# Performance work log

Measured on AMD Instinct MI355X. Metric: run time of the kernel, lower is better.

The kernel has to match this reference:

```python
import jax, jax.numpy as jnp
import numpy as np

B, LQ, LM, D, H = 2, 2048, 2048, 1024, 16
DH = D // H  # 64

def setup_inputs() -> dict:
    key = jax.random.key(0)
    ks = jax.random.split(key, 11)
    s = 0.02
    return {
        "query": jax.random.normal(ks[0], (B, LQ, D), jnp.float32),
        "memory": jax.random.normal(ks[1], (B, LM, D), jnp.float32),
        "memory_bias": jax.random.normal(ks[2], (B, LM), jnp.float32),
        "Wq": jax.random.normal(ks[3], (D, D), jnp.float32) * s,
        "bq": jnp.zeros((D,), jnp.float32),
        "Wk": jax.random.normal(ks[4], (D, D), jnp.float32) * s,
        "bk": jnp.zeros((D,), jnp.float32),
        "Wv": jax.random.normal(ks[5], (D, D), jnp.float32) * s,
        "bv": jnp.zeros((D,), jnp.float32),
        "Wo": jax.random.normal(ks[6], (D, D), jnp.float32) * s,
        "bo": jnp.zeros((D,), jnp.float32),
    }

def reference(query, memory, memory_bias, Wq, bq, Wk, bk, Wv, bv, Wo, bo):
    # QKV projections, split into heads: [B, L, H, DH]
    q = (query @ Wq + bq).reshape(B, LQ, H, DH)
    k = (memory @ Wk + bk).reshape(B, LM, H, DH)
    v = (memory @ Wv + bv).reshape(B, LM, H, DH)
    q = q * (DH ** -0.5)
    # logits: [B, H, Lq, Lk] (matches torch.einsum('btnh,bfnh->bnft', k, q))
    logits = jnp.einsum("bfnh,btnh->bnft", q, k)
    logits = logits + memory_bias[:, None, None, :]  # bias [B, Lm] -> [B,1,1,Lk]
    weights = jax.nn.softmax(logits, axis=-1)
    # dropout omitted (eval / rate 0 for correctness baseline)
    attn = jnp.einsum("bnft,btnh->bfnh", weights, v).reshape(B, LQ, D)
    return attn @ Wo + bo  # [B, Lq, output_depth]
```

## Files before the change

### kernel.cpp

```cpp
#include <hip/hip_runtime.h>
#include <hip/hip_bf16.h>
#include <math.h>


typedef __bf16 bf16;
typedef __bf16 bf16x4 __attribute__((ext_vector_type(4)));
typedef __bf16 bf16x8 __attribute__((ext_vector_type(8)));
typedef float f32x4 __attribute__((ext_vector_type(4)));

#define MFMA16(a, b, c) __builtin_amdgcn_mfma_f32_16x16x32_bf16((a), (b), (c), 0, 0, 0)

__device__ inline float exp2_hw(float x) {
    float r; asm("v_exp_f32 %0, %1" : "=v"(r) : "v"(x)); return r;
}

__device__ inline void gload_lds16(const void* g, void* l) {
    __builtin_amdgcn_global_load_lds(
        (const __attribute__((address_space(1))) void*)g,
        (__attribute__((address_space(3))) void*)l, 16, 0, 0);
}

__global__ __launch_bounds__(256) void prep_kernel(
    const float* __restrict__ query, const float* __restrict__ memory,
    const float* __restrict__ mbias,
    const float* __restrict__ W0, const float* __restrict__ W1,
    const float* __restrict__ W2, const float* __restrict__ W3,
    bf16* __restrict__ Yq, bf16* __restrict__ Ym, float* __restrict__ sbias,
    bf16* __restrict__ T0, bf16* __restrict__ T1,
    bf16* __restrict__ T2, bf16* __restrict__ T3)
{
    __shared__ float Ls[64][65];
    const int t = threadIdx.x;

    if (blockIdx.z == 0) {
        const float* X = blockIdx.y ? memory : query;
        bf16* Y = blockIdx.y ? Ym : Yq;
        const size_t i = ((size_t)blockIdx.x * 256 + t) * 8;
        float4 f0 = *(const float4*)&X[i];
        float4 f1 = *(const float4*)&X[i + 4];
        bf16x8 h;
        h[0] = (bf16)f0.x; h[1] = (bf16)f0.y; h[2] = (bf16)f0.z; h[3] = (bf16)f0.w;
        h[4] = (bf16)f1.x; h[5] = (bf16)f1.y; h[6] = (bf16)f1.z; h[7] = (bf16)f1.w;
        *(bf16x8*)&Y[i] = h;
        return;
    }
    const int x = blockIdx.x;
    if (x == 1024) {
        const int i = blockIdx.y * 2048 + t * 8;
        #pragma unroll
        for (int j = 0; j < 8; ++j) sbias[i + j] = mbias[i + j] * 1.44269504f;
        return;
    }
    if (x > 1024 || blockIdx.y) return;

    const int wsel = x >> 8, sub = x & 255;
    const float* W; bf16* T;
    switch (wsel) {
        case 0:  W = W0; T = T0; break;
        case 1:  W = W1; T = T1; break;
        case 2:  W = W2; T = T2; break;
        default: W = W3; T = T3; break;
    }
    const int n0 = (sub & 15) * 64, k0 = (sub >> 4) * 64;
    const int g = t >> 4, c = (t & 15) * 4;
    #pragma unroll
    for (int p = 0; p < 4; ++p) {
        const int row = p * 16 + g;
        float4 f = *(const float4*)&W[(size_t)(k0 + row) * 1024 + n0 + c];
        Ls[row][c + 0] = f.x; Ls[row][c + 1] = f.y;
        Ls[row][c + 2] = f.z; Ls[row][c + 3] = f.w;
    }
    __syncthreads();
    #pragma unroll
    for (int p = 0; p < 4; ++p) {
        const int n = p * 16 + g;
        bf16x4 h;
        h[0] = (bf16)Ls[c + 0][n]; h[1] = (bf16)Ls[c + 1][n];
        h[2] = (bf16)Ls[c + 2][n]; h[3] = (bf16)Ls[c + 3][n];
        *(bf16x4*)&T[(size_t)(n0 + n) * 1024 + k0 + c] = h;
    }
}

template <typename TO>
__global__ __launch_bounds__(256) void gemm_kernel(
    const bf16* __restrict__ A, const bf16* __restrict__ WT,
    const float* __restrict__ bias, TO* __restrict__ out,
    float alpha, int mode)
{
    __shared__ __align__(16) bf16 As[2][128 * 64];
    __shared__ __align__(16) bf16 Bs[2][64 * 64];

    const int fid = blockIdx.x + (blockIdx.y << 4);
    const int swz = (fid & 7) * 64 + (fid >> 3);
    const int n0 = (swz & 15) * 64;
    const int m0 = (swz >> 4) * 128;

    const int tid = threadIdx.x;
    const int w = tid >> 6, lane = tid & 63;
    const int lr = lane & 15, lg = lane >> 4;
    const int wm = (w >> 1) * 64, wn = (w & 1) * 32;

    const int arow0 = w * 32 + (lane >> 3);
    const int brow0 = w * 16 + (lane >> 3);
    const int sch = lane & 7;

    f32x4 acc[4][2] = {};

    auto stageG = [&](int kt, int bi) {
        #pragma unroll
        for (int p = 0; p < 4; ++p) {
            const int row = arow0 + p * 8;
            const int xc = ((sch ^ (row & 7)) << 3);
            gload_lds16(&A[(size_t)(m0 + row) * 1024 + kt + xc],
                        &As[bi][row * 64 + sch * 8]);
        }
        #pragma unroll
        for (int p = 0; p < 2; ++p) {
            const int row = brow0 + p * 8;
            const int xc = ((sch ^ (row & 7)) << 3);
            gload_lds16(&WT[(size_t)(n0 + row) * 1024 + kt + xc],
                        &Bs[bi][row * 64 + sch * 8]);
        }
    };

    stageG(0, 0);
    __syncthreads();

    int cur = 0;
    #pragma unroll 1
    for (int t = 0; t < 16; ++t) {
        if (t < 15) stageG((t + 1) * 64, cur ^ 1);

        #pragma unroll
        for (int ks = 0; ks < 2; ++ks) {
            const int c = (((ks * 4 + lg) ^ (lr & 7)) << 3);
            bf16x8 af[4], bfv[2];
            #pragma unroll
            for (int mt = 0; mt < 4; ++mt)
                af[mt] = *(const bf16x8*)&As[cur][(wm + mt * 16 + lr) * 64 + c];
            #pragma unroll
            for (int nt = 0; nt < 2; ++nt)
                bfv[nt] = *(const bf16x8*)&Bs[cur][(wn + nt * 16 + lr) * 64 + c];
            #pragma unroll
            for (int nt = 0; nt < 2; ++nt)
                #pragma unroll
                for (int mt = 0; mt < 4; ++mt)
                    acc[mt][nt] = MFMA16(af[mt], bfv[nt], acc[mt][nt]);
        }
        __syncthreads();
        cur ^= 1;
    }

    #pragma unroll
    for (int nt = 0; nt < 2; ++nt) {
        const int n = n0 + wn + nt * 16 + lr;
        const float bv = bias[n];
        #pragma unroll
        for (int mt = 0; mt < 4; ++mt) {
            #pragma unroll
            for (int i = 0; i < 4; ++i) {
                const int m = m0 + wm + mt * 16 + lg * 4 + i;
                const float v = (acc[mt][nt][i] + bv) * alpha;
                if (mode == 0) {
                    out[(size_t)m * 1024 + n] = (TO)v;
                } else {
                    const int b = m >> 11, t2 = m & 2047;
                    out[((size_t)(b << 10) + n) * 2048 + t2] = (TO)v;
                }
            }
        }
    }
}

__global__ __launch_bounds__(256) void gemm_kv_kernel(
    const bf16* __restrict__ A, const bf16* __restrict__ WTk,
    const bf16* __restrict__ WTv, const float* __restrict__ bk,
    const float* __restrict__ bv, bf16* __restrict__ Kout,
    bf16* __restrict__ Vtout)
{
    __shared__ __align__(16) bf16 As[2][128 * 64];
    __shared__ __align__(16) bf16 Bk[2][64 * 64];
    __shared__ __align__(16) bf16 Bv[2][64 * 64];

    const int fid = blockIdx.x + (blockIdx.y << 4);
    const int swz = (fid & 7) * 64 + (fid >> 3);
    const int n0 = (swz & 15) * 64;
    const int m0 = (swz >> 4) * 128;

    const int tid = threadIdx.x;
    const int w = tid >> 6, lane = tid & 63;
    const int lr = lane & 15, lg = lane >> 4;
    const int wm = (w >> 1) * 64, wn = (w & 1) * 32;

    const int arow0 = w * 32 + (lane >> 3);
    const int brow0 = w * 16 + (lane >> 3);
    const int sch = lane & 7;

    f32x4 accK[4][2] = {}, accV[4][2] = {};

    auto stageG = [&](int kt, int bi) {
        #pragma unroll
        for (int p = 0; p < 4; ++p) {
            const int row = arow0 + p * 8;
            const int xc = ((sch ^ (row & 7)) << 3);
            gload_lds16(&A[(size_t)(m0 + row) * 1024 + kt + xc],
                        &As[bi][row * 64 + sch * 8]);
        }
        #pragma unroll
        for (int p = 0; p < 2; ++p) {
            const int row = brow0 + p * 8;
            const int xc = ((sch ^ (row & 7)) << 3);
            gload_lds16(&WTk[(size_t)(n0 + row) * 1024 + kt + xc],
                        &Bk[bi][row * 64 + sch * 8]);
            gload_lds16(&WTv[(size_t)(n0 + row) * 1024 + kt + xc],
                        &Bv[bi][row * 64 + sch * 8]);
        }
    };

    stageG(0, 0);
    __syncthreads();

    int cur = 0;
    #pragma unroll 1
    for (int t = 0; t < 16; ++t) {
        if (t < 15) stageG((t + 1) * 64, cur ^ 1);

        #pragma unroll
        for (int ks = 0; ks < 2; ++ks) {
            const int c = (((ks * 4 + lg) ^ (lr & 7)) << 3);
            bf16x8 af[4], bkf[2], bvf[2];
            #pragma unroll
            for (int mt = 0; mt < 4; ++mt)
                af[mt] = *(const bf16x8*)&As[cur][(wm + mt * 16 + lr) * 64 + c];
            #pragma unroll
            for (int nt = 0; nt < 2; ++nt) {
                bkf[nt] = *(const bf16x8*)&Bk[cur][(wn + nt * 16 + lr) * 64 + c];
                bvf[nt] = *(const bf16x8*)&Bv[cur][(wn + nt * 16 + lr) * 64 + c];
            }
            #pragma unroll
            for (int nt = 0; nt < 2; ++nt)
                #pragma unroll
                for (int mt = 0; mt < 4; ++mt) {
                    accK[mt][nt] = MFMA16(af[mt], bkf[nt], accK[mt][nt]);
                    accV[mt][nt] = MFMA16(af[mt], bvf[nt], accV[mt][nt]);
                }
        }
        __syncthreads();
        cur ^= 1;
    }

    #pragma unroll
    for (int nt = 0; nt < 2; ++nt) {
        const int n = n0 + wn + nt * 16 + lr;
        const float bkv = bk[n], bvv = bv[n];
        #pragma unroll
        for (int mt = 0; mt < 4; ++mt) {
            #pragma unroll
            for (int i = 0; i < 4; ++i) {
                const int m = m0 + wm + mt * 16 + lg * 4 + i;
                Kout[(size_t)m * 1024 + n] = (bf16)(accK[mt][nt][i] + bkv);
                const int b = m >> 11, t2 = m & 2047;
                Vtout[((size_t)(b << 10) + n) * 2048 + t2] = (bf16)(accV[mt][nt][i] + bvv);
            }
        }
    }
}

__global__ __launch_bounds__(512) void attn_kernel(
    const bf16* __restrict__ Q, const bf16* __restrict__ K,
    const bf16* __restrict__ Vt, const float* __restrict__ sbias,
    bf16* __restrict__ Oout)
{
    __shared__ __align__(16) bf16 Kbuf[4][4096];
    __shared__ __align__(16) bf16 Vbuf[4][4096];
    __shared__ __align__(16) float Lbias[2048];

    const int tid = threadIdx.x;
    const int w = tid >> 6, lane = tid & 63;
    const int lr = lane & 15, lg = lane >> 4;

    const int fid = blockIdx.x + (blockIdx.y << 3) + (blockIdx.z << 7);
    const int swz = (fid & 7) * 32 + (fid >> 3);
    const int qt = swz & 7, head = (swz >> 3) & 15, b = swz >> 7;
    const int qrow = qt * 256 + w * 32;

    bf16x8 qf[2][2];
    #pragma unroll
    for (int g = 0; g < 2; ++g) {
        const size_t qo = (size_t)(b * 2048 + qrow + g * 16 + lr) * 1024 + head * 64;
        qf[g][0] = *(const bf16x8*)&Q[qo + lg * 8];
        qf[g][1] = *(const bf16x8*)&Q[qo + 32 + lg * 8];
    }

    const bf16* Kb = K + (size_t)b * 2048 * 1024 + head * 64;
    const bf16* Vb = Vt + ((size_t)b * 1024 + head * 64) * 2048;
    const float* biasb = sbias + b * 2048;

    float m_run[2] = {-INFINITY, -INFINITY};
    f32x4 of[2][4] = {};
    f32x4 ofl[2] = {};

    bf16x8 ones8;
    #pragma unroll
    for (int j = 0; j < 8; ++j) ones8[j] = (bf16)1.0f;

    const int R = tid >> 3, cc = tid & 7;
    const int cs = cc ^ (R & 7);
    const int piR = ((R & 16) << 1) | ((R & 12) << 1) | ((R & 32) >> 3) | (R & 3);
    auto stage = [&](int t, int slot) {
        gload_lds16(Kb + (size_t)(t * 64 + piR) * 1024 + cs * 8,
                    &Kbuf[slot][tid * 8]);
        gload_lds16(Vb + (size_t)R * 2048 + t * 64 + cs * 8,
                    &Vbuf[slot][tid * 8]);
    };

    stage(0, 0);
    stage(1, 1);
    gload_lds16(&biasb[tid * 4], &Lbias[tid * 4]);
    asm volatile("s_waitcnt vmcnt(0)" ::: "memory");
    __builtin_amdgcn_s_barrier();

    f32x4 b4[4];
    b4[0] = *(const f32x4*)&Lbias[8 * lg];
    b4[1] = *(const f32x4*)&Lbias[32 + 8 * lg];
    b4[2] = *(const f32x4*)&Lbias[4 + 8 * lg];
    b4[3] = *(const f32x4*)&Lbias[36 + 8 * lg];

    #pragma unroll 1
    for (int it = 0; it < 32; ++it) {
        const int slot = it & 3;
        stage(it < 30 ? it + 2 : 31, (it + 2) & 3);
        asm volatile("s_waitcnt vmcnt(4)" ::: "memory");
        __builtin_amdgcn_s_barrier();
        __builtin_amdgcn_sched_barrier(0);

        const int bt = ((it < 31) ? it + 1 : 31) * 64;
        f32x4 b4n[4];
        b4n[0] = *(const f32x4*)&Lbias[bt + 8 * lg];
        b4n[1] = *(const f32x4*)&Lbias[bt + 32 + 8 * lg];
        b4n[2] = *(const f32x4*)&Lbias[bt + 4 + 8 * lg];
        b4n[3] = *(const f32x4*)&Lbias[bt + 36 + 8 * lg];

        f32x4 s[2][4];
        #pragma unroll
        for (int g = 0; g < 2; ++g)
            #pragma unroll
            for (int nt = 0; nt < 4; ++nt) s[g][nt] = b4[nt];
        #pragma unroll
        for (int ks = 0; ks < 2; ++ks) {
            const int cw = (((ks * 4 + lg) ^ (lr & 7)) << 3);
            bf16x8 kf[4];
            #pragma unroll
            for (int nt = 0; nt < 4; ++nt)
                kf[nt] = *(const bf16x8*)&Kbuf[slot][(nt * 16 + lr) * 64 + cw];
            __builtin_amdgcn_s_setprio(1);
            #pragma unroll
            for (int nt = 0; nt < 4; ++nt) {
                s[0][nt] = MFMA16(kf[nt], qf[0][ks], s[0][nt]);
                s[1][nt] = MFMA16(kf[nt], qf[1][ks], s[1][nt]);
            }
            __builtin_amdgcn_s_setprio(0);
        }

        bf16x8 vf[2][4];
        #pragma unroll
        for (int ks = 0; ks < 2; ++ks) {
            const int cw = (((ks * 4 + lg) ^ (lr & 7)) << 3);
            #pragma unroll
            for (int dt = 0; dt < 4; ++dt)
                vf[ks][dt] = *(const bf16x8*)&Vbuf[slot][(dt * 16 + lr) * 64 + cw];
        }

        float rml[2];
        #pragma unroll
        for (int g = 0; g < 2; ++g) {
            float m0 = fmaxf(fmaxf(s[g][0][0], s[g][0][1]), fmaxf(s[g][0][2], s[g][0][3]));
            float m1 = fmaxf(fmaxf(s[g][1][0], s[g][1][1]), fmaxf(s[g][1][2], s[g][1][3]));
            float m2 = fmaxf(fmaxf(s[g][2][0], s[g][2][1]), fmaxf(s[g][2][2], s[g][2][3]));
            float m3 = fmaxf(fmaxf(s[g][3][0], s[g][3][1]), fmaxf(s[g][3][2], s[g][3][3]));
            rml[g] = fmaxf(fmaxf(m0, m1), fmaxf(m2, m3));
        }
        const bool need = (rml[0] > m_run[0] + 8.f) || (rml[1] > m_run[1] + 8.f);

        if (__any(need)) {
            #pragma unroll
            for (int g = 0; g < 2; ++g) {
                float mx = fmaxf(rml[g], __shfl_xor(rml[g], 16, 64));
                mx = fmaxf(mx, __shfl_xor(mx, 32, 64));
                const float mnew = fmaxf(m_run[g], mx);
                const float al = exp2_hw(m_run[g] - mnew);
                m_run[g] = mnew;
                ofl[g] *= al;
                #pragma unroll
                for (int dt = 0; dt < 4; ++dt) of[g][dt] *= al;
            }
        }

        bf16x8 pb[2][2];
        #pragma unroll
        for (int g = 0; g < 2; ++g)
            #pragma unroll
            for (int i = 0; i < 4; ++i) {
                pb[g][0][i]     = (bf16)exp2_hw(s[g][0][i] - m_run[g]);
                pb[g][1][i]     = (bf16)exp2_hw(s[g][1][i] - m_run[g]);
                pb[g][0][4 + i] = (bf16)exp2_hw(s[g][2][i] - m_run[g]);
                pb[g][1][4 + i] = (bf16)exp2_hw(s[g][3][i] - m_run[g]);
            }

        __builtin_amdgcn_s_setprio(1);
        #pragma unroll
        for (int ks = 0; ks < 2; ++ks) {
            #pragma unroll
            for (int g = 0; g < 2; ++g) {
                #pragma unroll
                for (int dt = 0; dt < 4; ++dt)
                    of[g][dt] = MFMA16(vf[ks][dt], pb[g][ks], of[g][dt]);
                ofl[g] = MFMA16(ones8, pb[g][ks], ofl[g]);
            }
        }
        __builtin_amdgcn_s_setprio(0);

        #pragma unroll
        for (int nt = 0; nt < 4; ++nt) b4[nt] = b4n[nt];
    }

    #pragma unroll
    for (int g = 0; g < 2; ++g) {
        const float inv = 1.0f / ofl[g][0];
        const size_t ob = (size_t)(b * 2048 + qrow + g * 16 + lr) * 1024 + head * 64;
        #pragma unroll
        for (int dt = 0; dt < 4; ++dt) {
            bf16x4 h4;
            #pragma unroll
            for (int i = 0; i < 4; ++i) h4[i] = (bf16)(of[g][dt][i] * inv);
            *(bf16x4*)&Oout[ob + dt * 16 + lg * 4] = h4;
        }
    }
}

extern "C" void kernel_launch(void* const* d_in, const int* in_sizes, int n_in,
                              void* d_out, int out_size, void* d_ws, size_t ws_size,
                              hipStream_t stream) {
    const float* query  = (const float*)d_in[0];
    const float* memory = (const float*)d_in[1];
    const float* mbias  = (const float*)d_in[2];
    const float* Wq = (const float*)d_in[3];
    const float* bq = (const float*)d_in[4];
    const float* Wk = (const float*)d_in[5];
    const float* bk = (const float*)d_in[6];
    const float* Wv = (const float*)d_in[7];
    const float* bv = (const float*)d_in[8];
    const float* Wo = (const float*)d_in[9];
    const float* bo = (const float*)d_in[10];
    float* out = (float*)d_out;

    const size_t SZ = 4096ull * 1024ull * sizeof(bf16);
    const size_t WZ = 1024ull * 1024ull * sizeof(bf16);
    char* ws = (char*)d_ws;
    bf16* Qp  = (bf16*)(ws);
    bf16* Kp  = (bf16*)(ws + SZ);
    bf16* Vtp = (bf16*)(ws + 2 * SZ);
    bf16* Ap  = (bf16*)(ws + 3 * SZ);
    bf16* WTq = (bf16*)(ws + 4 * SZ);
    bf16* WTk = (bf16*)(ws + 4 * SZ + WZ);
    bf16* WTv = (bf16*)(ws + 4 * SZ + 2 * WZ);
    bf16* WTo = (bf16*)(ws + 4 * SZ + 3 * WZ);
    float* sbias = (float*)(ws + 4 * SZ + 4 * WZ);

    dim3 blk(256);
    prep_kernel<<<dim3(2048, 2, 2), blk, 0, stream>>>(
        query, memory, mbias, Wq, Wk, Wv, Wo, Kp, Ap, sbias, WTq, WTk, WTv, WTo);

    dim3 gg(16, 32);
    gemm_kernel<bf16><<<gg, blk, 0, stream>>>(Kp, WTq, bq, Qp, 0.18033688f, 0);
    gemm_kv_kernel<<<gg, blk, 0, stream>>>(Ap, WTk, WTv, bk, bv, Kp, Vtp);
    attn_kernel<<<dim3(8, 16, 2), dim3(512), 0, stream>>>(Qp, Kp, Vtp, sbias, Ap);
    gemm_kernel<float><<<gg, blk, 0, stream>>>(Ap, WTo, bo, out, 1.0f, 0);
}
```

Measured before the change: 121.2 us.

## Fuse fp32-to-bf16 activation conversion into Q and KV projection GEMM loads

Removes the separate pass in the prep kernel that converted query and memory from fp32 to bf16. The Q and KV projection GEMMs now read fp32 activations directly through registers, convert them to bf16, and write them into swizzled LDS after the MFMA work of each k-step. This avoids writing and re-reading the bf16 activation copies in global memory. In exchange, A-tile loads go through VGPRs instead of direct-to-LDS loads, which raises register pressure, and each GEMM block reads twice as many bytes for A because multiple N-tiles re-read the fp32 rows.

```diff
diff --git a/kernel.cpp b/kernel.cpp
--- a/kernel.cpp
+++ b/kernel.cpp
@@ -21,37 +21,23 @@
 }
 
 __global__ __launch_bounds__(256) void prep_kernel(
-    const float* __restrict__ query, const float* __restrict__ memory,
     const float* __restrict__ mbias,
     const float* __restrict__ W0, const float* __restrict__ W1,
     const float* __restrict__ W2, const float* __restrict__ W3,
-    bf16* __restrict__ Yq, bf16* __restrict__ Ym, float* __restrict__ sbias,
+    float* __restrict__ sbias,
     bf16* __restrict__ T0, bf16* __restrict__ T1,
     bf16* __restrict__ T2, bf16* __restrict__ T3)
 {
     __shared__ float Ls[64][65];
     const int t = threadIdx.x;
-
-    if (blockIdx.z == 0) {
-        const float* X = blockIdx.y ? memory : query;
-        bf16* Y = blockIdx.y ? Ym : Yq;
-        const size_t i = ((size_t)blockIdx.x * 256 + t) * 8;
-        float4 f0 = *(const float4*)&X[i];
-        float4 f1 = *(const float4*)&X[i + 4];
-        bf16x8 h;
-        h[0] = (bf16)f0.x; h[1] = (bf16)f0.y; h[2] = (bf16)f0.z; h[3] = (bf16)f0.w;
-        h[4] = (bf16)f1.x; h[5] = (bf16)f1.y; h[6] = (bf16)f1.z; h[7] = (bf16)f1.w;
-        *(bf16x8*)&Y[i] = h;
+    const int x = blockIdx.x;
+
+    if (x == 1024) {
+        const int i = t * 16;
+        #pragma unroll
+        for (int j = 0; j < 16; ++j) sbias[i + j] = mbias[i + j] * 1.44269504f;
         return;
     }
-    const int x = blockIdx.x;
-    if (x == 1024) {
-        const int i = blockIdx.y * 2048 + t * 8;
-        #pragma unroll
-        for (int j = 0; j < 8; ++j) sbias[i + j] = mbias[i + j] * 1.44269504f;
-        return;
-    }
-    if (x > 1024 || blockIdx.y) return;
 
     const int wsel = x >> 8, sub = x & 255;
     const float* W; bf16* T;
@@ -82,8 +68,8 @@
 }
 
 template <typename TO>
-__global__ __launch_bounds__(256) void gemm_kernel(
-    const bf16* __restrict__ A, const bf16* __restrict__ WT,
+__global__ __launch_bounds__(256) void gemm_f32a_kernel(
+    const float* __restrict__ A, const bf16* __restrict__ WT,
     const float* __restrict__ bias, TO* __restrict__ out,
     float alpha, int mode)
 {
@@ -100,20 +86,32 @@
     const int lr = lane & 15, lg = lane >> 4;
     const int wm = (w >> 1) * 64, wn = (w & 1) * 32;
 
-    const int arow0 = w * 32 + (lane >> 3);
+    const int ar = tid >> 1;
+    const int ac = (tid & 1) * 32;
     const int brow0 = w * 16 + (lane >> 3);
     const int sch = lane & 7;
 
     f32x4 acc[4][2] = {};
-
-    auto stageG = [&](int kt, int bi) {
-        #pragma unroll
-        for (int p = 0; p < 4; ++p) {
-            const int row = arow0 + p * 8;
-            const int xc = ((sch ^ (row & 7)) << 3);
-            gload_lds16(&A[(size_t)(m0 + row) * 1024 + kt + xc],
-                        &As[bi][row * 64 + sch * 8]);
-        }
+    float4 fa[8];
+
+    auto issueA = [&](int kt) {
+        const float* src = &A[(size_t)(m0 + ar) * 1024 + kt + ac];
+        #pragma unroll
+        for (int j = 0; j < 8; ++j) fa[j] = *(const float4*)&src[j * 4];
+    };
+    auto writeA = [&](int bi) {
+        #pragma unroll
+        for (int j = 0; j < 4; ++j) {
+            bf16x8 h;
+            h[0] = (bf16)fa[2*j].x;   h[1] = (bf16)fa[2*j].y;
+            h[2] = (bf16)fa[2*j].z;   h[3] = (bf16)fa[2*j].w;
+            h[4] = (bf16)fa[2*j+1].x; h[5] = (bf16)fa[2*j+1].y;
+            h[6] = (bf16)fa[2*j+1].z; h[7] = (bf16)fa[2*j+1].w;
+            const int wc = ((ac >> 3) + j) ^ (ar & 7);
+            *(bf16x8*)&As[bi][ar * 64 + wc * 8] = h;
+        }
+    };
+    auto stageB = [&](int kt, int bi) {
         #pragma unroll
         for (int p = 0; p < 2; ++p) {
             const int row = brow0 + p * 8;
@@ -123,13 +121,15 @@
         }
     };
 
-    stageG(0, 0);
+    issueA(0);
+    stageB(0, 0);
+    writeA(0);
     __syncthreads();
 
     int cur = 0;
     #pragma unroll 1
     for (int t = 0; t < 16; ++t) {
-        if (t < 15) stageG((t + 1) * 64, cur ^ 1);
+        if (t < 15) { issueA((t + 1) * 64); stageB((t + 1) * 64, cur ^ 1); }
 
         #pragma unroll
         for (int ks = 0; ks < 2; ++ks) {
@@ -147,6 +147,7 @@
                 for (int mt = 0; mt < 4; ++mt)
                     acc[mt][nt] = MFMA16(af[mt], bfv[nt], acc[mt][nt]);
         }
+        if (t < 15) writeA(cur ^ 1);
         __syncthreads();
         cur ^= 1;
     }
@@ -172,8 +173,8 @@
     }
 }
 
-__global__ __launch_bounds__(256) void gemm_kv_kernel(
-    const bf16* __restrict__ A, const bf16* __restrict__ WTk,
+__global__ __launch_bounds__(256) void gemm_kv_f32a_kernel(
+    const float* __restrict__ A, const bf16* __restrict__ WTk,
     const bf16* __restrict__ WTv, const float* __restrict__ bk,
     const float* __restrict__ bv, bf16* __restrict__ Kout,
     bf16* __restrict__ Vtout)
@@ -192,20 +193,32 @@
     const int lr = lane & 15, lg = lane >> 4;
     const int wm = (w >> 1) * 64, wn = (w & 1) * 32;
 
-    const int arow0 = w * 32 + (lane >> 3);
+    const int ar = tid >> 1;
+    const int ac = (tid & 1) * 32;
     const int brow0 = w * 16 + (lane >> 3);
     const int sch = lane & 7;
 
     f32x4 accK[4][2] = {}, accV[4][2] = {};
-
-    auto stageG = [&](int kt, int bi) {
-        #pragma unroll
-        for (int p = 0; p < 4; ++p) {
-            const int row = arow0 + p * 8;
-            const int xc = ((sch ^ (row & 7)) << 3);
-            gload_lds16(&A[(size_t)(m0 + row) * 1024 + kt + xc],
-                        &As[bi][row * 64 + sch * 8]);
-        }
+    float4 fa[8];
+
+    auto issueA = [&](int kt) {
+        const float* src = &A[(size_t)(m0 + ar) * 1024 + kt + ac];
+        #pragma unroll
+        for (int j = 0; j < 8; ++j) fa[j] = *(const float4*)&src[j * 4];
+    };
+    auto writeA = [&](int bi) {
+        #pragma unroll
+        for (int j = 0; j < 4; ++j) {
+            bf16x8 h;
+            h[0] = (bf16)fa[2*j].x;   h[1] = (bf16)fa[2*j].y;
+            h[2] = (bf16)fa[2*j].z;   h[3] = (bf16)fa[2*j].w;
+            h[4] = (bf16)fa[2*j+1].x; h[5] = (bf16)fa[2*j+1].y;
+            h[6] = (bf16)fa[2*j+1].z; h[7] = (bf16)fa[2*j+1].w;
+            const int wc = ((ac >> 3) + j) ^ (ar & 7);
+            *(bf16x8*)&As[bi][ar * 64 + wc * 8] = h;
+        }
+    };
+    auto stageB = [&](int kt, int bi) {
         #pragma unroll
         for (int p = 0; p < 2; ++p) {
             const int row = brow0 + p * 8;
@@ -217,13 +230,15 @@
         }
     };
 
-    stageG(0, 0);
+    issueA(0);
+    stageB(0, 0);
+    writeA(0);
     __syncthreads();
 
     int cur = 0;
     #pragma unroll 1
     for (int t = 0; t < 16; ++t) {
-        if (t < 15) stageG((t + 1) * 64, cur ^ 1);
+        if (t < 15) { issueA((t + 1) * 64); stageB((t + 1) * 64, cur ^ 1); }
 
         #pragma unroll
         for (int ks = 0; ks < 2; ++ks) {
@@ -245,6 +260,7 @@
                     accV[mt][nt] = MFMA16(af[mt], bvf[nt], accV[mt][nt]);
                 }
         }
+        if (t < 15) writeA(cur ^ 1);
         __syncthreads();
         cur ^= 1;
     }
@@ -261,6 +277,97 @@
                 Kout[(size_t)m * 1024 + n] = (bf16)(accK[mt][nt][i] + bkv);
                 const int b = m >> 11, t2 = m & 2047;
                 Vtout[((size_t)(b << 10) + n) * 2048 + t2] = (bf16)(accV[mt][nt][i] + bvv);
+            }
+        }
+    }
+}
+
+template <typename TO>
+__global__ __launch_bounds__(256) void gemm_kernel(
+    const bf16* __restrict__ A, const bf16* __restrict__ WT,
+    const float* __restrict__ bias, TO* __restrict__ out,
+    float alpha, int mode)
+{
+    __shared__ __align__(16) bf16 As[2][128 * 64];
+    __shared__ __align__(16) bf16 Bs[2][64 * 64];
+
+    const int fid = blockIdx.x + (blockIdx.y << 4);
+    const int swz = (fid & 7) * 64 + (fid >> 3);
+    const int n0 = (swz & 15) * 64;
+    const int m0 = (swz >> 4) * 128;
+
+    const int tid = threadIdx.x;
+    const int w = tid >> 6, lane = tid & 63;
+    const int lr = lane & 15, lg = lane >> 4;
+    const int wm = (w >> 1) * 64, wn = (w & 1) * 32;
+
+    const int arow0 = w * 32 + (lane >> 3);
+    const int brow0 = w * 16 + (lane >> 3);
+    const int sch = lane & 7;
+
+    f32x4 acc[4][2] = {};
+
+    auto stageG = [&](int kt, int bi) {
+        #pragma unroll
+        for (int p = 0; p < 4; ++p) {
+            const int row = arow0 + p * 8;
+            const int xc = ((sch ^ (row & 7)) << 3);
+            gload_lds16(&A[(size_t)(m0 + row) * 1024 + kt + xc],
+                        &As[bi][row * 64 + sch * 8]);
+        }
+        #pragma unroll
+        for (int p = 0; p < 2; ++p) {
+            const int row = brow0 + p * 8;
+            const int xc = ((sch ^ (row & 7)) << 3);
+            gload_lds16(&WT[(size_t)(n0 + row) * 1024 + kt + xc],
+                        &Bs[bi][row * 64 + sch * 8]);
+        }
+    };
+
+    stageG(0, 0);
+    __syncthreads();
+
+    int cur = 0;
+    #pragma unroll 1
+    for (int t = 0; t < 16; ++t) {
+        if (t < 15) stageG((t + 1) * 64, cur ^ 1);
+
+        #pragma unroll
+        for (int ks = 0; ks < 2; ++ks) {
+            const int c = (((ks * 4 + lg) ^ (lr & 7)) << 3);
+            bf16x8 af[4], bfv[2];
+            #pragma unroll
+            for (int mt = 0; mt < 4; ++mt)
+                af[mt] = *(const bf16x8*)&As[cur][(wm + mt * 16 + lr) * 64 + c];
+            #pragma unroll
+            for (int nt = 0; nt < 2; ++nt)
+                bfv[nt] = *(const bf16x8*)&Bs[cur][(wn + nt * 16 + lr) * 64 + c];
+            #pragma unroll
+            for (int nt = 0; nt < 2; ++nt)
+                #pragma unroll
+                for (int mt = 0; mt < 4; ++mt)
+                    acc[mt][nt] = MFMA16(af[mt], bfv[nt], acc[mt][nt]);
+        }
+        __syncthreads();
+        cur ^= 1;
+    }
+
+    #pragma unroll
+    for (int nt = 0; nt < 2; ++nt) {
+        const int n = n0 + wn + nt * 16 + lr;
+        const float bv = bias[n];
+        #pragma unroll
+        for (int mt = 0; mt < 4; ++mt) {
+            #pragma unroll
+            for (int i = 0; i < 4; ++i) {
+                const int m = m0 + wm + mt * 16 + lg * 4 + i;
+                const float v = (acc[mt][nt][i] + bv) * alpha;
+                if (mode == 0) {
+                    out[(size_t)m * 1024 + n] = (TO)v;
+                } else {
+                    const int b = m >> 11, t2 = m & 2047;
+                    out[((size_t)(b << 10) + n) * 2048 + t2] = (TO)v;
+                }
             }
         }
     }
@@ -468,12 +575,12 @@
     float* sbias = (float*)(ws + 4 * SZ + 4 * WZ);
 
     dim3 blk(256);
-    prep_kernel<<<dim3(2048, 2, 2), blk, 0, stream>>>(
-        query, memory, mbias, Wq, Wk, Wv, Wo, Kp, Ap, sbias, WTq, WTk, WTv, WTo);
+    prep_kernel<<<dim3(1025), blk, 0, stream>>>(
+        mbias, Wq, Wk, Wv, Wo, sbias, WTq, WTk, WTv, WTo);
 
     dim3 gg(16, 32);
-    gemm_kernel<bf16><<<gg, blk, 0, stream>>>(Kp, WTq, bq, Qp, 0.18033688f, 0);
-    gemm_kv_kernel<<<gg, blk, 0, stream>>>(Ap, WTk, WTv, bk, bv, Kp, Vtp);
+    gemm_f32a_kernel<bf16><<<gg, blk, 0, stream>>>(query, WTq, bq, Qp, 0.18033688f, 0);
+    gemm_kv_f32a_kernel<<<gg, blk, 0, stream>>>(memory, WTk, WTv, bk, bv, Kp, Vtp);
     attn_kernel<<<dim3(8, 16, 2), dim3(512), 0, stream>>>(Qp, Kp, Vtp, sbias, Ap);
     gemm_kernel<float><<<gg, blk, 0, stream>>>(Ap, WTo, bo, out, 1.0f, 0);
 }
```

Result: slower. 160.1 us (+32.1%).
